# Optimization experiments

Hardware: AMD Instinct MI355X
Metric: run time of the kernel (lower is better)

The kernel has to match this reference:

```python
import jax, jax.numpy as jnp
import numpy as np

B, H, W = 4, 496, 496
M = 8  # max vertices of a quad-quad convex intersection


def _corners(boxes):
    # boxes [..., 7] = (x, y, z, dx, dy, dz, heading) -> CCW BEV corners [..., 4, 2]
    x, y, dx, dy, r = boxes[..., 0], boxes[..., 1], boxes[..., 3], boxes[..., 4], boxes[..., 6]
    lx = jnp.array([0.5, -0.5, -0.5, 0.5], dtype=boxes.dtype) * dx[..., None]
    ly = jnp.array([0.5, 0.5, -0.5, -0.5], dtype=boxes.dtype) * dy[..., None]
    c, s = jnp.cos(r)[..., None], jnp.sin(r)[..., None]
    cx = x[..., None] + c * lx - s * ly
    cy = y[..., None] + s * lx + c * ly
    return jnp.stack([cx, cy], axis=-1)


def _clip(poly, cnt, a, b):
    # Clip padded CCW polygon (poly [M,2], cnt valid verts) by halfplane left of edge a->b.
    idx = jnp.arange(M)
    valid = idx < cnt
    nidx = jnp.where(idx + 1 >= cnt, 0, idx + 1)
    cur, nxt = poly, poly[nidx]
    ex, ey = b[0] - a[0], b[1] - a[1]
    dc = ex * (cur[:, 1] - a[1]) - ey * (cur[:, 0] - a[0])  # signed dist of cur
    dn = ex * (nxt[:, 1] - a[1]) - ey * (nxt[:, 0] - a[0])
    inc, inn = dc >= 0, dn >= 0
    keep = inc & valid                      # emit cur if inside
    crs = (inc != inn) & valid              # emit edge/line intersection if crossing
    den = dc - dn
    t = dc / jnp.where(jnp.abs(den) < 1e-9, 1.0, den)
    ip = cur + t[:, None] * (nxt - cur)
    c = keep.astype(jnp.int32) + crs.astype(jnp.int32)
    offs = jnp.cumsum(c) - c                # exclusive prefix sum -> output slots
    out = jnp.zeros_like(poly)
    out = out.at[jnp.where(keep, offs, M)].set(cur, mode='drop')
    out = out.at[jnp.where(crs, offs + keep.astype(jnp.int32), M)].set(ip, mode='drop')
    return out, jnp.sum(c)


def _inter_area(ca, cb):
    # Intersection area of two CCW quads (each [4,2]) via Sutherland-Hodgman.
    poly = jnp.zeros((M, 2), ca.dtype).at[:4].set(ca)
    cnt = jnp.int32(4)
    for i in range(4):
        poly, cnt = _clip(poly, cnt, cb[i], cb[(i + 1) % 4])
    idx = jnp.arange(M)
    valid = idx < cnt
    nidx = jnp.where(idx + 1 >= cnt, 0, idx + 1)
    nxt = poly[nidx]
    cr = poly[:, 0] * nxt[:, 1] - nxt[:, 0] * poly[:, 1]  # shoelace terms
    return 0.5 * jnp.abs(jnp.sum(jnp.where(valid, cr, 0.0)))


def _iou3d_aligned(boxes_a, boxes_b):
    # Element-wise (aligned) 3D oriented-box IoU. boxes [N,7] -> iou [N].
    inter_bev = jax.vmap(_inter_area)(_corners(boxes_a), _corners(boxes_b))
    za0, za1 = boxes_a[:, 2] - 0.5 * boxes_a[:, 5], boxes_a[:, 2] + 0.5 * boxes_a[:, 5]
    zb0, zb1 = boxes_b[:, 2] - 0.5 * boxes_b[:, 5], boxes_b[:, 2] + 0.5 * boxes_b[:, 5]
    zo = jnp.maximum(jnp.minimum(za1, zb1) - jnp.maximum(za0, zb0), 0.0)
    inter_vol = inter_bev * zo
    vol_a = boxes_a[:, 3] * boxes_a[:, 4] * boxes_a[:, 5]
    vol_b = boxes_b[:, 3] * boxes_b[:, 4] * boxes_b[:, 5]
    return inter_vol / (vol_a + vol_b - inter_vol + 1e-7)


def setup_inputs() -> dict:
    key = jax.random.key(0)
    kc, kd, kr, kn, km, kp, ki = jax.random.split(key, 7)
    center = jax.random.normal(kc, (B, H, W, 3), dtype=jnp.float32) * 2.0
    dims = jax.random.uniform(kd, (B, H, W, 3), minval=0.5, maxval=3.0, dtype=jnp.float32)
    heading = jax.random.uniform(kr, (B, H, W, 1), minval=-np.pi, maxval=np.pi, dtype=jnp.float32)
    box_gt = jnp.concatenate([center, dims, heading], axis=-1)  # [B,H,W,7]
    pred = box_gt + jax.random.normal(kn, box_gt.shape, dtype=jnp.float32) * 0.1
    pred = pred.at[..., 3:6].set(jnp.maximum(pred[..., 3:6], 0.2))  # keep dims positive
    box_pred = jnp.transpose(pred, (0, 3, 1, 2))  # [B,7,H,W]
    mask = jax.random.randint(km, (B, H, W), 0, 2, dtype=jnp.int32)
    iou_pred = jax.random.normal(kp, (B, H, W), dtype=jnp.float32) * 0.5
    ind = jax.random.randint(ki, (B, 128), 0, H * W, dtype=jnp.int32)  # unused by the layer
    return {"iou_pred": iou_pred, "mask": mask, "ind": ind, "box_pred": box_pred, "box_gt": box_gt}


def reference(iou_pred, mask, ind, box_pred, box_gt):
    pred = jnp.transpose(box_pred, (0, 2, 3, 1)).reshape(-1, 7)  # [N,7]
    gt = box_gt.reshape(-1, 7)
    target = 2.0 * _iou3d_aligned(pred, gt) - 1.0               # [N]
    m = mask.astype(jnp.float32).reshape(-1)
    loss = jnp.sum(m * jnp.abs(iou_pred.reshape(-1) - target))
    return loss / (jnp.sum(m) + 1e-4)
```

## Files before the change

### kernel.cpp

```cpp
#include <hip/hip_runtime.h>
#include <math.h>

#define B_   4
#define H_   496
#define W_   496
#define HW_  (H_ * W_)
#define N_   (B_ * HW_)
#define TPB  256
#define NPT  4
#define EPB  (TPB * NPT)
#define NBLK (N_ / EPB)

static_assert(N_ % EPB == 0, "no tail");
static_assert(HW_ % NPT == 0, "thread quad must not straddle batch b");

union F4 { float4 v; float a[4]; };
union I4 { int4 v; int a[4]; };

__device__ __forceinline__ float edge_delta(float xk, float yk,
                                            float dx, float dy,
                                            float rdx, float rdy,
                                            float hx, float hy) {
    float t0 = 0.f, t1 = 1.f, tl;
    tl = __builtin_amdgcn_fmed3f((hy - yk) * rdy, 0.f, 1.f);
    t0 = fmaxf(t0, (dy < 0.f) ? tl : 0.f);
    t1 = fminf(t1, (dy > 0.f) ? tl : 1.f);
    tl = __builtin_amdgcn_fmed3f(-(xk + hx) * rdx, 0.f, 1.f);
    t0 = fmaxf(t0, (dx > 0.f) ? tl : 0.f);
    t1 = fminf(t1, (dx < 0.f) ? tl : 1.f);
    tl = __builtin_amdgcn_fmed3f(-(yk + hy) * rdy, 0.f, 1.f);
    t0 = fmaxf(t0, (dy > 0.f) ? tl : 0.f);
    t1 = fminf(t1, (dy < 0.f) ? tl : 1.f);
    tl = __builtin_amdgcn_fmed3f((hx - xk) * rdx, 0.f, 1.f);
    t0 = fmaxf(t0, (dx < 0.f) ? tl : 0.f);
    t1 = fminf(t1, (dx > 0.f) ? tl : 1.f);
    return fmaxf(t1 - t0, 0.f);
}

__device__ __forceinline__ void iou_elem(
    float pax, float pay, float paz, float pdx, float pdy, float pdz, float pr,
    float gax, float gay, float gaz, float gdx, float gdy, float gdz, float gr,
    float ip, float m, float& num, float& den)
{
    float sp, cp; __sincosf(pr, &sp, &cp);
    float sg, cg; __sincosf(gr, &sg, &cg);
    const float cth = fmaf(cp, cg,  sp * sg);
    const float sth = fmaf(sp, cg, -cp * sg);
    const float wx = pax - gax, wy = pay - gay;
    const float cx = fmaf(cg, wx,  sg * wy);
    const float cy = fmaf(cg, wy, -sg * wx);

    const float phx = 0.5f * pdx, phy = 0.5f * pdy;
    const float ghx = 0.5f * gdx, ghy = 0.5f * gdy;

    const float a1 = cth * phx, b1 = sth * phx;
    const float a2 = sth * phy, b2 = cth * phy;
    const float e1 = a1 - a2, e2 = a1 + a2;
    const float f1 = b1 + b2, f2 = b1 - b2;
    const float px0 = cx + e1, py0 = cy + f1;
    const float px1 = cx - e2, py1 = cy - f2;
    const float px2 = cx - e1, py2 = cy - f1;
    const float px3 = cx + e2, py3 = cy + f2;

    const float ta1 = a1 + a1, tb1 = b1 + b1;
    const float ta2 = a2 + a2, tb2 = b2 + b2;
    const float ra1 = __builtin_amdgcn_rcpf(ta1);
    const float rb1 = __builtin_amdgcn_rcpf(tb1);
    const float ra2 = __builtin_amdgcn_rcpf(ta2);
    const float rb2 = __builtin_amdgcn_rcpf(tb2);

    float inter;
    {
        const float d0 = edge_delta(px0, py0, -ta1, -tb1, -ra1, -rb1, ghx, ghy);
        const float d1 = edge_delta(px1, py1,  ta2, -tb2,  ra2, -rb2, ghx, ghy);
        const float d2 = edge_delta(px2, py2,  ta1,  tb1,  ra1,  rb1, ghx, ghy);
        const float d3 = edge_delta(px3, py3, -ta2,  tb2, -ra2,  rb2, ghx, ghy);
        inter =        d0 * fmaf(a1, py0, -b1 * px0);
        inter = fmaf(  d1, -fmaf(b2, px1,  a2 * py1), inter);
        inter = fmaf(  d2,  fmaf(b1, px2, -a1 * py2), inter);
        inter = fmaf(  d3,  fmaf(b2, px3,  a2 * py3), inter);
    }

    {
        const float A  = cth * ghx, Dv = sth * ghx;
        const float Bq = sth * ghy, Ev = cth * ghy;
        const float Cc = fmaf(cth, cx,  sth * cy);
        const float Gf = fmaf(sth, cx, -cth * cy);
        const float g1 = A + Bq,  g2 = A - Bq;
        const float h1 = Ev - Dv, h2 = Ev + Dv;
        const float u0 =  g1 - Cc, v0 =  h1 + Gf;
        const float u1 = -g2 - Cc, v1 =  h2 + Gf;
        const float u2 = -g1 - Cc, v2 = -h1 + Gf;
        const float u3 =  g2 - Cc, v3 = -h2 + Gf;

        const float tA = A + A,   tD = Dv + Dv;
        const float tB = Bq + Bq, tE = Ev + Ev;
        const float rA = __builtin_amdgcn_rcpf(tA);
        const float rD = __builtin_amdgcn_rcpf(tD);
        const float rB = __builtin_amdgcn_rcpf(tB);
        const float rE = __builtin_amdgcn_rcpf(tE);

        float sq;
        sq  = edge_delta(u0, v0, -tA,  tD, -rA,  rD, phx, phy);
        sq += edge_delta(u1, v1, -tB, -tE, -rB, -rE, phx, phy);
        sq += edge_delta(u2, v2,  tA, -tD,  rA, -rD, phx, phy);
        sq += edge_delta(u3, v3,  tB,  tE,  rB,  rE, phx, phy);
        inter = fmaf(ghx * ghy, sq, inter);
    }

    const float za0 = paz - 0.5f * pdz, za1 = paz + 0.5f * pdz;
    const float zb0 = gaz - 0.5f * gdz, zb1 = gaz + 0.5f * gdz;
    const float zo  = fmaxf(fminf(za1, zb1) - fmaxf(za0, zb0), 0.f);
    const float iv  = inter * zo;
    const float va  = pdx * pdy * pdz;
    const float vb  = gdx * gdy * gdz;
    const float iou = __fdividef(iv, va + vb - iv + 1e-7f);
    const float target = 2.f * iou - 1.f;

    num = fmaf(m, fabsf(ip - target), num);
    den += m;
}

__global__ __launch_bounds__(TPB) void iou_main(
    const float* __restrict__ iou_pred,
    const int*   __restrict__ mask,
    const float* __restrict__ box_pred,
    const float* __restrict__ box_gt,
    float2* __restrict__ ws)
{
    __shared__ float rn[4], rd[4];

    const int tid = threadIdx.x;
    const int n0  = (blockIdx.x * TPB + tid) * NPT;
    const int b   = n0 / HW_;
    const int hw  = n0 - b * HW_;

    const float* bp = box_pred + (size_t)b * 7 * HW_ + hw;
    F4 pc[7];
#pragma unroll
    for (int c = 0; c < 7; ++c)
        pc[c].v = *(const float4*)(bp + (size_t)c * HW_);

    float gtv[28];
    {
        const float4* g4 = (const float4*)(box_gt + (size_t)n0 * 7);
#pragma unroll
        for (int j = 0; j < 7; ++j)
            *(float4*)(gtv + 4 * j) = g4[j];
    }
    F4 ip4; ip4.v = *(const float4*)(iou_pred + n0);
    I4 mk4; mk4.v = *(const int4*)(mask + n0);

    float num = 0.f, den = 0.f;
#pragma unroll
    for (int e = 0; e < NPT; ++e) {
        const float* g = gtv + 7 * e;
        iou_elem(pc[0].a[e], pc[1].a[e], pc[2].a[e],
                 pc[3].a[e], pc[4].a[e], pc[5].a[e], pc[6].a[e],
                 g[0], g[1], g[2], g[3], g[4], g[5], g[6],
                 ip4.a[e], (float)mk4.a[e], num, den);
    }

#pragma unroll
    for (int off = 32; off > 0; off >>= 1) {
        num += __shfl_down(num, off);
        den += __shfl_down(den, off);
    }
    if ((tid & 63) == 0) { rn[tid >> 6] = num; rd[tid >> 6] = den; }
    __syncthreads();
    if (tid == 0)
        ws[blockIdx.x] = make_float2(rn[0] + rn[1] + rn[2] + rn[3],
                                     rd[0] + rd[1] + rd[2] + rd[3]);
}

__global__ __launch_bounds__(TPB) void iou_fin(const float2* __restrict__ ws,
                                               float* __restrict__ out) {
    __shared__ float rn[4], rd[4];
    float sn = 0.f, sd = 0.f;
    for (int i = threadIdx.x; i < NBLK; i += TPB) {
        const float2 v = ws[i];
        sn += v.x;
        sd += v.y;
    }
#pragma unroll
    for (int off = 32; off > 0; off >>= 1) {
        sn += __shfl_down(sn, off);
        sd += __shfl_down(sd, off);
    }
    const int tid = threadIdx.x;
    if ((tid & 63) == 0) { rn[tid >> 6] = sn; rd[tid >> 6] = sd; }
    __syncthreads();
    if (tid == 0)
        out[0] = (rn[0] + rn[1] + rn[2] + rn[3]) /
                 (rd[0] + rd[1] + rd[2] + rd[3] + 1e-4f);
}

extern "C" void kernel_launch(void* const* d_in, const int* in_sizes, int n_in,
                              void* d_out, int out_size, void* d_ws, size_t ws_size,
                              hipStream_t stream) {
    const float* iou_pred = (const float*)d_in[0];
    const int*   mask     = (const int*)  d_in[1];
    const float* box_pred = (const float*)d_in[3];
    const float* box_gt   = (const float*)d_in[4];
    float*  out = (float*)d_out;
    float2* ws  = (float2*)d_ws;

    iou_main<<<NBLK, TPB, 0, stream>>>(iou_pred, mask, box_pred, box_gt, ws);
    iou_fin<<<1, TPB, 0, stream>>>(ws, out);
}
```

Baseline: 105.6 us.

## Fuse final reduction into main kernel via last-block spin-wait on checksummed records

```diff
diff --git a/kernel.cpp b/kernel.cpp
--- a/kernel.cpp
+++ b/kernel.cpp
@@ -121,12 +121,13 @@
     den += m;
 }
 
-__global__ __launch_bounds__(TPB) void iou_main(
+__global__ __launch_bounds__(TPB) void iou_fused(
     const float* __restrict__ iou_pred,
     const int*   __restrict__ mask,
     const float* __restrict__ box_pred,
     const float* __restrict__ box_gt,
-    float2* __restrict__ ws)
+    unsigned int* __restrict__ ws,
+    float* __restrict__ out)
 {
     __shared__ float rn[4], rd[4];
 
@@ -168,26 +169,43 @@
     }
     if ((tid & 63) == 0) { rn[tid >> 6] = num; rd[tid >> 6] = den; }
     __syncthreads();
-    if (tid == 0)
-        ws[blockIdx.x] = make_float2(rn[0] + rn[1] + rn[2] + rn[3],
-                                     rd[0] + rd[1] + rd[2] + rd[3]);
-}
-
-__global__ __launch_bounds__(TPB) void iou_fin(const float2* __restrict__ ws,
-                                               float* __restrict__ out) {
-    __shared__ float rn[4], rd[4];
+
+    if (blockIdx.x != NBLK - 1) {
+        if (tid == 0) {
+            const unsigned int a = __float_as_uint(rn[0] + rn[1] + rn[2] + rn[3]);
+            const unsigned int bb = __float_as_uint(rd[0] + rd[1] + rd[2] + rd[3]);
+            unsigned int* rec = ws + 4u * blockIdx.x;
+            __hip_atomic_store(rec + 0,  a, __ATOMIC_RELAXED, __HIP_MEMORY_SCOPE_AGENT);
+            __hip_atomic_store(rec + 1, bb, __ATOMIC_RELAXED, __HIP_MEMORY_SCOPE_AGENT);
+            __hip_atomic_store(rec + 2, ~a, __ATOMIC_RELAXED, __HIP_MEMORY_SCOPE_AGENT);
+            __hip_atomic_store(rec + 3, ~bb, __ATOMIC_RELAXED, __HIP_MEMORY_SCOPE_AGENT);
+        }
+        return;
+    }
+
     float sn = 0.f, sd = 0.f;
-    for (int i = threadIdx.x; i < NBLK; i += TPB) {
-        const float2 v = ws[i];
-        sn += v.x;
-        sd += v.y;
-    }
+    if (tid == 0) { sn = rn[0] + rn[1] + rn[2] + rn[3];
+                    sd = rd[0] + rd[1] + rd[2] + rd[3]; }
+    for (int i = tid; i < NBLK - 1; i += TPB) {
+        const unsigned int* rec = ws + 4u * i;
+        unsigned int a, bb, c, d;
+        for (;;) {
+            a  = __hip_atomic_load(rec + 0, __ATOMIC_RELAXED, __HIP_MEMORY_SCOPE_AGENT);
+            c  = __hip_atomic_load(rec + 2, __ATOMIC_RELAXED, __HIP_MEMORY_SCOPE_AGENT);
+            bb = __hip_atomic_load(rec + 1, __ATOMIC_RELAXED, __HIP_MEMORY_SCOPE_AGENT);
+            d  = __hip_atomic_load(rec + 3, __ATOMIC_RELAXED, __HIP_MEMORY_SCOPE_AGENT);
+            if ((c == ~a) && (d == ~bb)) break;
+            __builtin_amdgcn_s_sleep(2);
+        }
+        sn += __uint_as_float(a);
+        sd += __uint_as_float(bb);
+    }
+    __syncthreads();
 #pragma unroll
     for (int off = 32; off > 0; off >>= 1) {
         sn += __shfl_down(sn, off);
         sd += __shfl_down(sd, off);
     }
-    const int tid = threadIdx.x;
     if ((tid & 63) == 0) { rn[tid >> 6] = sn; rd[tid >> 6] = sd; }
     __syncthreads();
     if (tid == 0)
@@ -202,9 +220,8 @@
     const int*   mask     = (const int*)  d_in[1];
     const float* box_pred = (const float*)d_in[3];
     const float* box_gt   = (const float*)d_in[4];
-    float*  out = (float*)d_out;
-    float2* ws  = (float2*)d_ws;
-
-    iou_main<<<NBLK, TPB, 0, stream>>>(iou_pred, mask, box_pred, box_gt, ws);
-    iou_fin<<<1, TPB, 0, stream>>>(ws, out);
-}
+    float*        out = (float*)d_out;
+    unsigned int* ws  = (unsigned int*)d_ws;
+
+    iou_fused<<<NBLK, TPB, 0, stream>>>(iou_pred, mask, box_pred, box_gt, ws, out);
+}
```

Result: no change. 104.7 us (-0.9%).
